# Kernel tuning notes

Measured on AMD Instinct MI355X. Metric: run time of the kernel, lower is better.

The kernel has to match this reference:

```python
import jax, jax.numpy as jnp
import numpy as np

B, DIM, H, W = 4, 512, 64, 64
HEADS = 8
MAX_FREQ = 10000.0


def _rope_cos_sin(h, w, head_dim, dtype):
    # 2D RoPE: first quarter of half_dim uses row position, second quarter uses col position
    half = head_dim // 2
    quarter = half // 2
    pos_h = jnp.arange(h, dtype=dtype)
    pos_w = jnp.arange(w, dtype=dtype)
    gh, gw = jnp.meshgrid(pos_h, pos_w, indexing='ij')
    pos = jnp.stack([gh.ravel(), gw.ravel()], axis=-1)  # [N, 2]
    freqs = 1.0 / (MAX_FREQ ** (jnp.arange(quarter, dtype=dtype) / quarter))  # [quarter]
    ang_x = pos[:, 0:1] * freqs  # [N, quarter]
    ang_y = pos[:, 1:2] * freqs  # [N, quarter]
    cos = jnp.concatenate([jnp.cos(ang_x), jnp.cos(ang_y)], axis=-1)  # [N, half]
    sin = jnp.concatenate([jnp.sin(ang_x), jnp.sin(ang_y)], axis=-1)  # [N, half]
    return cos, sin


def _apply_rope(x, cos, sin):
    # x: [B, heads, N, head_dim]; cos/sin: [N, head_dim//2]
    d = x.shape[-1] // 2
    x1, x2 = x[..., :d], x[..., d:]
    return jnp.concatenate([x1 * cos - x2 * sin, x1 * sin + x2 * cos], axis=-1)


def setup_inputs() -> dict:
    key = jax.random.key(0)
    kx, kq, kp = jax.random.split(key, 3)
    x = jax.random.normal(kx, (B, DIM, H, W), dtype=jnp.float32)
    w_qkv = jax.random.normal(kq, (3 * DIM, DIM), dtype=jnp.float32) * (DIM ** -0.5)
    w_proj = jax.random.normal(kp, (DIM, DIM), dtype=jnp.float32) * (DIM ** -0.5)
    return {"x": x, "w_qkv": w_qkv, "w_proj": w_proj}


def reference(x, w_qkv, w_proj):
    Bb, C, Hh, Ww = x.shape
    heads = HEADS
    hd = C // heads
    N = Hh * Ww
    # 1x1 conv (bias-free) == channel-wise linear
    qkv = jnp.einsum('bchw,oc->bohw', x, w_qkv)  # [B, 3C, H, W]
    qkv = qkv.reshape(Bb, 3, heads, hd, Hh, Ww).transpose(1, 0, 2, 4, 5, 3)  # [3, B, heads, H, W, hd]
    q = qkv[0].reshape(Bb, heads, N, hd)
    k = qkv[1].reshape(Bb, heads, N, hd)
    v = qkv[2].reshape(Bb, heads, N, hd)
    cos, sin = _rope_cos_sin(Hh, Ww, hd, x.dtype)
    q = _apply_rope(q, cos, sin)
    k = _apply_rope(k, cos, sin)
    scale = hd ** -0.5
    attn = jax.nn.softmax(jnp.einsum('bhnd,bhmd->bhnm', q, k) * scale, axis=-1)  # [B, heads, N, N]
    out = jnp.einsum('bhnm,bhmd->bhnd', attn, v)  # [B, heads, N, hd]
    out = out.reshape(Bb, heads, Hh, Ww, hd).transpose(0, 1, 4, 2, 3).reshape(Bb, C, Hh, Ww)
    return jnp.einsum('bchw,oc->bohw', out, w_proj)
```

## Files before the change

### kernel.cpp

```cpp
#include <hip/hip_runtime.h>
#include <math.h>

#define B_    4
#define CDIM  512
#define HEADS 8
#define HD    64
#define NN    4096
#define QSZ   ((size_t)B_*HEADS*NN*HD)
#define SCALE_Q 0.18033688011112042f

typedef __attribute__((ext_vector_type(8))) short short8;
typedef __attribute__((ext_vector_type(4))) float f32x4;
typedef __attribute__((ext_vector_type(16))) float f32x16;
union U4S8 { uint4 u; short8 s; };

__device__ inline unsigned pk(float a, float b) {
    unsigned ua = __float_as_uint(a), ub = __float_as_uint(b);
    ua += 0x7FFFu + ((ua >> 16) & 1u);
    ub += 0x7FFFu + ((ub >> 16) & 1u);
    return (ua >> 16) | (ub & 0xFFFF0000u);
}
__device__ inline unsigned short bf16_1(float a) {
    unsigned ua = __float_as_uint(a);
    ua += 0x7FFFu + ((ua >> 16) & 1u);
    return (unsigned short)(ua >> 16);
}
__device__ inline unsigned cvtpk(float a, float b) {
    unsigned r;
    asm("v_cvt_pk_bf16_f32 %0, %1, %2" : "=v"(r) : "v"(a), "v"(b));
    return r;
}

__device__ inline void load_lds16(const unsigned short* g, unsigned short* l) {
    __builtin_amdgcn_global_load_lds(
        (const __attribute__((address_space(1))) unsigned int*)g,
        (__attribute__((address_space(3))) unsigned int*)l, 16, 0, 0);
}

__global__ void conv_w_kernel(const float* __restrict__ wq, const float* __restrict__ wp,
                              unsigned short* __restrict__ wqb, unsigned short* __restrict__ wpb) {
    int id = blockIdx.x * 256 + threadIdx.x;
    const float* src; unsigned short* dst; size_t off; float sc = 1.0f;
    if (id < 98304) { src = wq; dst = wqb; off = (size_t)id * 8; if (off < 262144) sc = SCALE_Q; }
    else            { src = wp; dst = wpb; off = (size_t)(id - 98304) * 8; }
    float4 a = *(const float4*)(src + off);
    float4 b = *(const float4*)(src + off + 4);
    uint4 u;
    u.x = pk(a.x * sc, a.y * sc); u.y = pk(a.z * sc, a.w * sc);
    u.z = pk(b.x * sc, b.y * sc); u.w = pk(b.z * sc, b.w * sc);
    *(uint4*)(dst + off) = u;
}

__global__ void rope_table_kernel(float* __restrict__ ct, float* __restrict__ st) {
    int id = blockIdx.x * 256 + threadIdx.x;
    int j = id >> 12, n = id & 4095;
    int i = j & 15;
    float pos = (j < 16) ? (float)(n >> 6) : (float)(n & 63);
    float freq = exp2f(-(float)i * 0.8304820237218406f);
    float ang = pos * freq;
    ct[id] = cosf(ang);
    st[id] = sinf(ang);
}

__global__ __launch_bounds__(256) void transpose_x_kernel(
        const float* __restrict__ x, unsigned short* __restrict__ xt) {
    __shared__ unsigned short T[64 * 72];
    int t = threadIdx.x;
    int b = blockIdx.z, c0 = blockIdx.y * 64, n0 = blockIdx.x * 64;
    const float* xb = x + ((size_t)b * CDIM + c0) * NN + n0;
    int crow = t >> 2, nseg = t & 3;
#pragma unroll
    for (int g = 0; g < 4; ++g) {
        float4 f = *(const float4*)(xb + (size_t)crow * NN + nseg * 16 + g * 4);
        int nb = nseg * 16 + g * 4;
        T[(nb + 0) * 72 + crow] = bf16_1(f.x);
        T[(nb + 1) * 72 + crow] = bf16_1(f.y);
        T[(nb + 2) * 72 + crow] = bf16_1(f.z);
        T[(nb + 3) * 72 + crow] = bf16_1(f.w);
    }
    __syncthreads();
    unsigned short* xo = xt + ((size_t)b * NN + n0) * CDIM + c0;
    int nrow = t >> 2, cseg = t & 3;
    uint4 u0 = *(uint4*)(T + nrow * 72 + cseg * 16);
    uint4 u1 = *(uint4*)(T + nrow * 72 + cseg * 16 + 8);
    *(uint4*)(xo + (size_t)nrow * CDIM + cseg * 16)     = u0;
    *(uint4*)(xo + (size_t)nrow * CDIM + cseg * 16 + 8) = u1;
}

__global__ __launch_bounds__(256, 2) void qkv_mfma_kernel(
        const unsigned short* __restrict__ xt, const unsigned short* __restrict__ wq,
        unsigned short* __restrict__ qbf, unsigned short* __restrict__ kbf,
        unsigned short* __restrict__ vt,
        const float* __restrict__ ct, const float* __restrict__ st) {
    __shared__ unsigned short smem[8192];
    int t = threadIdx.x;
    int lane = t & 63, w = t >> 6;
    int qlo = lane & 15, quad = lane >> 4;
    int b = blockIdx.z, o0 = blockIdx.y * 128, n0 = blockIdx.x * 128;
    const unsigned short* xb = xt + (size_t)b * NN * CDIM;
    int row = t >> 2, seg = t & 3;
    int wn = (w & 1) * 64, wo = (w >> 1) * 64;

    f32x4 acc[4][4];
#pragma unroll
    for (int i = 0; i < 4; ++i)
#pragma unroll
        for (int j = 0; j < 4; ++j) acc[i][j] = f32x4{0.f, 0.f, 0.f, 0.f};

    for (int k0 = 0; k0 < 512; k0 += 32) {
        __syncthreads();
        load_lds16(xb + (size_t)(n0 + row) * 512 + k0 + seg * 8,        smem + t * 8);
        load_lds16(xb + (size_t)(n0 + 64 + row) * 512 + k0 + seg * 8,   smem + 2048 + t * 8);
        load_lds16(wq + (size_t)(o0 + row) * 512 + k0 + seg * 8,        smem + 4096 + t * 8);
        load_lds16(wq + (size_t)(o0 + 64 + row) * 512 + k0 + seg * 8,   smem + 6144 + t * 8);
        __syncthreads();
        U4S8 af[4], bf[4];
#pragma unroll
        for (int mt = 0; mt < 4; ++mt)
            af[mt].u = *(const uint4*)(smem + (wn + 16 * mt + qlo) * 32 + quad * 8);
#pragma unroll
        for (int nt = 0; nt < 4; ++nt)
            bf[nt].u = *(const uint4*)(smem + 4096 + (wo + 16 * nt + qlo) * 32 + quad * 8);
#pragma unroll
        for (int mt = 0; mt < 4; ++mt)
#pragma unroll
            for (int nt = 0; nt < 4; ++nt)
                acc[mt][nt] = __builtin_amdgcn_mfma_f32_16x16x32_bf16(
                    af[mt].s, bf[nt].s, acc[mt][nt], 0, 0, 0);
    }

    int og = o0 + wo;
    int s = og >> 9;
    int h = (og & 511) >> 6;
    int bh = b * HEADS + h;
    if (s < 2) {
        unsigned short* dst = (s ? kbf : qbf) + (size_t)bh * NN * HD;
#pragma unroll
        for (int mt = 0; mt < 4; ++mt) {
            int nbase = n0 + wn + 16 * mt + 4 * quad;
#pragma unroll
            for (int ntp = 0; ntp < 2; ++ntp) {
                int j = 16 * ntp + qlo;
                float4 c4 = *(const float4*)(ct + (size_t)j * NN + nbase);
                float4 s4 = *(const float4*)(st + (size_t)j * NN + nbase);
                float cc[4] = {c4.x, c4.y, c4.z, c4.w};
                float ss[4] = {s4.x, s4.y, s4.z, s4.w};
#pragma unroll
                for (int r = 0; r < 4; ++r) {
                    float x1 = acc[mt][ntp][r], x2 = acc[mt][ntp + 2][r];
                    size_t base = (size_t)(nbase + r) * HD;
                    dst[base + j]      = bf16_1(x1 * cc[r] - x2 * ss[r]);
                    dst[base + j + 32] = bf16_1(x1 * ss[r] + x2 * cc[r]);
                }
            }
        }
    } else {
        unsigned short* dst = vt + (size_t)bh * HD * NN;
#pragma unroll
        for (int mt = 0; mt < 4; ++mt)
#pragma unroll
            for (int nt = 0; nt < 4; ++nt) {
                int d = 16 * nt + qlo;
                int n = n0 + wn + 16 * mt + 4 * quad;
                uint2 u;
                u.x = pk(acc[mt][nt][0], acc[mt][nt][1]);
                u.y = pk(acc[mt][nt][2], acc[mt][nt][3]);
                *(uint2*)(dst + (size_t)d * NN + n) = u;
            }
    }
}

__global__ __launch_bounds__(256, 2) void attn_kernel(
        const unsigned short* __restrict__ qbf, const unsigned short* __restrict__ kbf,
        const unsigned short* __restrict__ vt, unsigned short* __restrict__ aot) {
    __shared__ unsigned char smem[18432];
    int t = threadIdx.x;
    int lane = t & 63, w = t >> 6;
    int l31 = lane & 31, h = lane >> 5;
    int bb = blockIdx.z, hh = blockIdx.y;
    int bh = bb * HEADS + hh;
    int n0w = blockIdx.x * 256 + w * 64;

    U4S8 qf[2][4];
    const unsigned short* qg = qbf + ((size_t)bh * NN + n0w) * HD;
#pragma unroll
    for (int mtq = 0; mtq < 2; ++mtq)
#pragma unroll
        for (int ks = 0; ks < 4; ++ks)
            qf[mtq][ks].u = *(const uint4*)(qg + (size_t)(32 * mtq + l31) * 64 + 16 * ks + 8 * h);

    short8 vone;
#pragma unroll
    for (int i = 0; i < 8; ++i) vone[i] = (short)0x3F80;

    f32x16 Zv;
#pragma unroll
    for (int i = 0; i < 16; ++i) Zv[i] = 0.f;

    f32x16 O[2][2];
#pragma unroll
    for (int mtq = 0; mtq < 2; ++mtq)
#pragma unroll
        for (int ntd = 0; ntd < 2; ++ntd) O[mtq][ntd] = Zv;
    f32x16 Lacc[2];
    Lacc[0] = Zv; Lacc[1] = Zv;

    const uint4* kg = (const uint4*)kbf + (size_t)bh * NN * 8;
    const uint4* vg = (const uint4*)vt  + (size_t)bh * 64 * 512;

    int rr0 = t >> 3, s8 = t & 7;
    int voff = 32 * (s8 >> 1) + 8 * (s8 & 1);
    uint4 kr0, kr1, vr0, vr1;
    kr0 = kg[(size_t)rr0 * 8 + s8];
    kr1 = kg[(size_t)(32 + rr0) * 8 + s8];
    vr0 = vg[(size_t)rr0 * 512 + s8];
    vr1 = vg[(size_t)(32 + rr0) * 512 + s8];

    for (int c = 0; c < NN / 64; ++c) {
        __syncthreads();
        *(uint4*)(smem + rr0 * 144 + s8 * 16)        = kr0;
        *(uint4*)(smem + (32 + rr0) * 144 + s8 * 16) = kr1;
        *(uint2*)(smem + 9216 + rr0 * 144 + voff)             = make_uint2(vr0.x, vr0.y);
        *(uint2*)(smem + 9216 + rr0 * 144 + voff + 16)        = make_uint2(vr0.z, vr0.w);
        *(uint2*)(smem + 9216 + (32 + rr0) * 144 + voff)      = make_uint2(vr1.x, vr1.y);
        *(uint2*)(smem + 9216 + (32 + rr0) * 144 + voff + 16) = make_uint2(vr1.z, vr1.w);
        __syncthreads();
        if (c + 1 < NN / 64) {
            int m0 = (c + 1) * 64;
            kr0 = kg[(size_t)(m0 + rr0) * 8 + s8];
            kr1 = kg[(size_t)(m0 + 32 + rr0) * 8 + s8];
            vr0 = vg[(size_t)rr0 * 512 + (m0 >> 3) + s8];
            vr1 = vg[(size_t)(32 + rr0) * 512 + (m0 >> 3) + s8];
        }

#pragma unroll
        for (int mtk = 0; mtk < 2; ++mtk) {
            U4S8 ka[4];
#pragma unroll
            for (int ks = 0; ks < 4; ++ks)
                ka[ks].u = *(const uint4*)(smem + (32 * mtk + l31) * 144 + 32 * ks + 16 * h);
            f32x16 S[2];
            __builtin_amdgcn_s_setprio(1);
#pragma unroll
            for (int mtq = 0; mtq < 2; ++mtq) {
                S[mtq] = __builtin_amdgcn_mfma_f32_32x32x16_bf16(
                    ka[0].s, qf[mtq][0].s, Zv, 0, 0, 0);
#pragma unroll
                for (int ks = 1; ks < 4; ++ks)
                    S[mtq] = __builtin_amdgcn_mfma_f32_32x32x16_bf16(
                        ka[ks].s, qf[mtq][ks].s, S[mtq], 0, 0, 0);
            }
            __builtin_amdgcn_s_setprio(0);

            U4S8 pa[2][2];
#pragma unroll
            for (int mtq = 0; mtq < 2; ++mtq) {
                float p[16];
#pragma unroll
                for (int r = 0; r < 16; ++r) p[r] = __builtin_amdgcn_exp2f(S[mtq][r]);
#pragma unroll
                for (int ksl = 0; ksl < 2; ++ksl) {
                    pa[ksl][mtq].u.x = cvtpk(p[8 * ksl + 0], p[8 * ksl + 1]);
                    pa[ksl][mtq].u.y = cvtpk(p[8 * ksl + 2], p[8 * ksl + 3]);
                    pa[ksl][mtq].u.z = cvtpk(p[8 * ksl + 4], p[8 * ksl + 5]);
                    pa[ksl][mtq].u.w = cvtpk(p[8 * ksl + 6], p[8 * ksl + 7]);
                }
            }

            __builtin_amdgcn_s_setprio(1);
#pragma unroll
            for (int ksl = 0; ksl < 2; ++ksl) {
#pragma unroll
                for (int mtq = 0; mtq < 2; ++mtq)
                    Lacc[mtq] = __builtin_amdgcn_mfma_f32_32x32x16_bf16(
                        pa[ksl][mtq].s, vone, Lacc[mtq], 0, 0, 0);
#pragma unroll
                for (int ntd = 0; ntd < 2; ++ntd) {
                    U4S8 vb;
                    vb.u = *(const uint4*)(smem + 9216 + (32 * ntd + l31) * 144
                                           + 64 * mtk + 32 * ksl + 16 * h);
#pragma unroll
                    for (int mtq = 0; mtq < 2; ++mtq)
                        O[mtq][ntd] = __builtin_amdgcn_mfma_f32_32x32x16_bf16(
                            pa[ksl][mtq].s, vb.s, O[mtq][ntd], 0, 0, 0);
                }
            }
            __builtin_amdgcn_s_setprio(0);
        }
    }

    __syncthreads();
    unsigned short* Tw = (unsigned short*)(smem + w * 4608);
    unsigned short* aob = aot + ((size_t)bb * NN) * CDIM + hh * 64;
#pragma unroll
    for (int mtq = 0; mtq < 2; ++mtq) {
        float iv[16];
#pragma unroll
        for (int r = 0; r < 16; ++r) iv[r] = 1.0f / Lacc[mtq][r];
#pragma unroll
        for (int rg = 0; rg < 2; ++rg) {
#pragma unroll
            for (int ntd = 0; ntd < 2; ++ntd)
#pragma unroll
                for (int rr = 0; rr < 8; ++rr) {
                    int r = 8 * rg + rr;
                    int q16 = (rr & 3) + 8 * (rr >> 2) + 4 * h;
                    Tw[q16 * 72 + 32 * ntd + l31] = bf16_1(O[mtq][ntd][r] * iv[r]);
                }
            int row = lane >> 2, cseg = lane & 3;
            uint4 u0 = *(uint4*)(Tw + row * 72 + cseg * 16);
            uint4 u1 = *(uint4*)(Tw + row * 72 + cseg * 16 + 8);
            unsigned short* arow = aob
                + (size_t)(n0w + 32 * mtq + 16 * rg + row) * CDIM + cseg * 16;
            *(uint4*)(arow)     = u0;
            *(uint4*)(arow + 8) = u1;
        }
    }
}

__global__ __launch_bounds__(256, 2) void proj_mfma_kernel(
        const unsigned short* __restrict__ aot, const unsigned short* __restrict__ wp,
        float* __restrict__ out) {
    __shared__ unsigned short smem[8192];
    int t = threadIdx.x;
    int lane = t & 63, w = t >> 6;
    int qlo = lane & 15, quad = lane >> 4;
    int b = blockIdx.z, o0 = blockIdx.y * 128, n0 = blockIdx.x * 128;
    const unsigned short* ab = aot + (size_t)b * NN * CDIM;
    int row = t >> 2, seg = t & 3;
    int wn = (w & 1) * 64, wo = (w >> 1) * 64;

    f32x4 acc[4][4];
#pragma unroll
    for (int i = 0; i < 4; ++i)
#pragma unroll
        for (int j = 0; j < 4; ++j) acc[i][j] = f32x4{0.f, 0.f, 0.f, 0.f};

    for (int k0 = 0; k0 < 512; k0 += 32) {
        __syncthreads();
        load_lds16(ab + (size_t)(n0 + row) * 512 + k0 + seg * 8,        smem + t * 8);
        load_lds16(ab + (size_t)(n0 + 64 + row) * 512 + k0 + seg * 8,   smem + 2048 + t * 8);
        load_lds16(wp + (size_t)(o0 + row) * 512 + k0 + seg * 8,        smem + 4096 + t * 8);
        load_lds16(wp + (size_t)(o0 + 64 + row) * 512 + k0 + seg * 8,   smem + 6144 + t * 8);
        __syncthreads();
        U4S8 af[4], bf[4];
#pragma unroll
        for (int mt = 0; mt < 4; ++mt)
            af[mt].u = *(const uint4*)(smem + (wn + 16 * mt + qlo) * 32 + quad * 8);
#pragma unroll
        for (int nt = 0; nt < 4; ++nt)
            bf[nt].u = *(const uint4*)(smem + 4096 + (wo + 16 * nt + qlo) * 32 + quad * 8);
#pragma unroll
        for (int mt = 0; mt < 4; ++mt)
#pragma unroll
            for (int nt = 0; nt < 4; ++nt)
                acc[mt][nt] = __builtin_amdgcn_mfma_f32_16x16x32_bf16(
                    af[mt].s, bf[nt].s, acc[mt][nt], 0, 0, 0);
    }

    float* ob = out + (size_t)b * CDIM * NN;
#pragma unroll
    for (int mt = 0; mt < 4; ++mt)
#pragma unroll
        for (int nt = 0; nt < 4; ++nt) {
            int o = o0 + wo + 16 * nt + qlo;
            int n = n0 + wn + 16 * mt + 4 * quad;
            *(float4*)(ob + (size_t)o * NN + n) = *(float4*)&acc[mt][nt];
        }
}

extern "C" void kernel_launch(void* const* d_in, const int* in_sizes, int n_in,
                              void* d_out, int out_size, void* d_ws, size_t ws_size,
                              hipStream_t stream) {
    const float* x      = (const float*)d_in[0];
    const float* w_qkv  = (const float*)d_in[1];
    const float* w_proj = (const float*)d_in[2];
    float* out = (float*)d_out;
    unsigned short* ws = (unsigned short*)d_ws;

    unsigned short* xt  = ws;
    unsigned short* qbf = xt  + QSZ;
    unsigned short* kbf = qbf + QSZ;
    unsigned short* vt  = kbf + QSZ;
    unsigned short* aot = vt  + QSZ;
    unsigned short* wqb = aot + QSZ;
    unsigned short* wpb = wqb + 786432;
    float* ct = (float*)(wpb + 262144);
    float* st = ct + 32 * 4096;

    conv_w_kernel<<<512, 256, 0, stream>>>(w_qkv, w_proj, wqb, wpb);
    rope_table_kernel<<<512, 256, 0, stream>>>(ct, st);
    transpose_x_kernel<<<dim3(64, 8, B_), 256, 0, stream>>>(x, xt);
    qkv_mfma_kernel<<<dim3(32, 12, B_), 256, 0, stream>>>(xt, wqb, qbf, kbf, vt, ct, st);
    attn_kernel<<<dim3(NN / 256, HEADS, B_), 256, 0, stream>>>(qbf, kbf, vt, aot);
    proj_mfma_kernel<<<dim3(32, 4, B_), 256, 0, stream>>>(aot, wpb, out);
}
```

Measured before the change: 293.7 us.

## Replace ones-vector MFMA row-sum with scalar accumulation and restructure S tile loop

Removes the MFMA that multiplied P by a ones vector to get the softmax denominator. Each lane now sums its exp values in scalar registers, combines halves with a cross-lane shuffle at the end, and redistributes the reciprocals to the output row layout via shuffles. The QK^T loop is also reordered to compute both key sub-tiles (S[2][2]) at once before exp and PV. This cuts matrix-core work per tile, but adds VALU adds, uses the fp32 rather than bf16-rounded P for the sum, and keeps more live registers.

```diff
diff --git a/kernel.cpp b/kernel.cpp
--- a/kernel.cpp
+++ b/kernel.cpp
@@ -189,10 +189,6 @@
         for (int ks = 0; ks < 4; ++ks)
             qf[mtq][ks].u = *(const uint4*)(qg + (size_t)(32 * mtq + l31) * 64 + 16 * ks + 8 * h);
 
-    short8 vone;
-#pragma unroll
-    for (int i = 0; i < 8; ++i) vone[i] = (short)0x3F80;
-
     f32x16 Zv;
 #pragma unroll
     for (int i = 0; i < 16; ++i) Zv[i] = 0.f;
@@ -202,8 +198,7 @@
     for (int mtq = 0; mtq < 2; ++mtq)
 #pragma unroll
         for (int ntd = 0; ntd < 2; ++ntd) O[mtq][ntd] = Zv;
-    f32x16 Lacc[2];
-    Lacc[0] = Zv; Lacc[1] = Zv;
+    float Lsum[2] = {0.f, 0.f};
 
     const uint4* kg = (const uint4*)kbf + (size_t)bh * NN * 8;
     const uint4* vg = (const uint4*)vt  + (size_t)bh * 64 * 512;
@@ -233,47 +228,62 @@
             vr1 = vg[(size_t)(32 + rr0) * 512 + (m0 >> 3) + s8];
         }
 
-#pragma unroll
-        for (int mtk = 0; mtk < 2; ++mtk) {
-            U4S8 ka[4];
-#pragma unroll
-            for (int ks = 0; ks < 4; ++ks)
-                ka[ks].u = *(const uint4*)(smem + (32 * mtk + l31) * 144 + 32 * ks + 16 * h);
-            f32x16 S[2];
-            __builtin_amdgcn_s_setprio(1);
-#pragma unroll
-            for (int mtq = 0; mtq < 2; ++mtq) {
-                S[mtq] = __builtin_amdgcn_mfma_f32_32x32x16_bf16(
-                    ka[0].s, qf[mtq][0].s, Zv, 0, 0, 0);
-#pragma unroll
-                for (int ks = 1; ks < 4; ++ks)
-                    S[mtq] = __builtin_amdgcn_mfma_f32_32x32x16_bf16(
-                        ka[ks].s, qf[mtq][ks].s, S[mtq], 0, 0, 0);
+        f32x16 S[2][2];
+        __builtin_amdgcn_s_setprio(1);
+        {
+            U4S8 ka0[2];
+#pragma unroll
+            for (int mtk = 0; mtk < 2; ++mtk)
+                ka0[mtk].u = *(const uint4*)(smem + (32 * mtk + l31) * 144 + 16 * h);
+#pragma unroll
+            for (int mtk = 0; mtk < 2; ++mtk)
+#pragma unroll
+                for (int mtq = 0; mtq < 2; ++mtq)
+                    S[mtk][mtq] = __builtin_amdgcn_mfma_f32_32x32x16_bf16(
+                        ka0[mtk].s, qf[mtq][0].s, Zv, 0, 0, 0);
+#pragma unroll
+            for (int ks = 1; ks < 4; ++ks) {
+                U4S8 ka[2];
+#pragma unroll
+                for (int mtk = 0; mtk < 2; ++mtk)
+                    ka[mtk].u = *(const uint4*)(smem + (32 * mtk + l31) * 144 + 32 * ks + 16 * h);
+#pragma unroll
+                for (int mtk = 0; mtk < 2; ++mtk)
+#pragma unroll
+                    for (int mtq = 0; mtq < 2; ++mtq)
+                        S[mtk][mtq] = __builtin_amdgcn_mfma_f32_32x32x16_bf16(
+                            ka[mtk].s, qf[mtq][ks].s, S[mtk][mtq], 0, 0, 0);
             }
-            __builtin_amdgcn_s_setprio(0);
-
-            U4S8 pa[2][2];
-#pragma unroll
-            for (int mtq = 0; mtq < 2; ++mtq) {
-                float p[16];
-#pragma unroll
-                for (int r = 0; r < 16; ++r) p[r] = __builtin_amdgcn_exp2f(S[mtq][r]);
+        }
+        __builtin_amdgcn_s_setprio(0);
+
+        U4S8 pa[2][2][2];
+#pragma unroll
+        for (int mtk = 0; mtk < 2; ++mtk)
+#pragma unroll
+            for (int mtq = 0; mtq < 2; ++mtq)
 #pragma unroll
                 for (int ksl = 0; ksl < 2; ++ksl) {
-                    pa[ksl][mtq].u.x = cvtpk(p[8 * ksl + 0], p[8 * ksl + 1]);
-                    pa[ksl][mtq].u.y = cvtpk(p[8 * ksl + 2], p[8 * ksl + 3]);
-                    pa[ksl][mtq].u.z = cvtpk(p[8 * ksl + 4], p[8 * ksl + 5]);
-                    pa[ksl][mtq].u.w = cvtpk(p[8 * ksl + 6], p[8 * ksl + 7]);
+                    float p0 = __builtin_amdgcn_exp2f(S[mtk][mtq][8 * ksl + 0]);
+                    float p1 = __builtin_amdgcn_exp2f(S[mtk][mtq][8 * ksl + 1]);
+                    float p2 = __builtin_amdgcn_exp2f(S[mtk][mtq][8 * ksl + 2]);
+                    float p3 = __builtin_amdgcn_exp2f(S[mtk][mtq][8 * ksl + 3]);
+                    float p4 = __builtin_amdgcn_exp2f(S[mtk][mtq][8 * ksl + 4]);
+                    float p5 = __builtin_amdgcn_exp2f(S[mtk][mtq][8 * ksl + 5]);
+                    float p6 = __builtin_amdgcn_exp2f(S[mtk][mtq][8 * ksl + 6]);
+                    float p7 = __builtin_amdgcn_exp2f(S[mtk][mtq][8 * ksl + 7]);
+                    Lsum[mtq] += ((p0 + p1) + (p2 + p3)) + ((p4 + p5) + (p6 + p7));
+                    pa[mtk][ksl][mtq].u.x = cvtpk(p0, p1);
+                    pa[mtk][ksl][mtq].u.y = cvtpk(p2, p3);
+                    pa[mtk][ksl][mtq].u.z = cvtpk(p4, p5);
+                    pa[mtk][ksl][mtq].u.w = cvtpk(p6, p7);
                 }
-            }
-
-            __builtin_amdgcn_s_setprio(1);
-#pragma unroll
-            for (int ksl = 0; ksl < 2; ++ksl) {
-#pragma unroll
-                for (int mtq = 0; mtq < 2; ++mtq)
-                    Lacc[mtq] = __builtin_amdgcn_mfma_f32_32x32x16_bf16(
-                        pa[ksl][mtq].s, vone, Lacc[mtq], 0, 0, 0);
+
+        __builtin_amdgcn_s_setprio(1);
+#pragma unroll
+        for (int mtk = 0; mtk < 2; ++mtk)
+#pragma unroll
+            for (int ksl = 0; ksl < 2; ++ksl)
 #pragma unroll
                 for (int ntd = 0; ntd < 2; ++ntd) {
                     U4S8 vb;
@@ -282,13 +292,17 @@
 #pragma unroll
                     for (int mtq = 0; mtq < 2; ++mtq)
                         O[mtq][ntd] = __builtin_amdgcn_mfma_f32_32x32x16_bf16(
-                            pa[ksl][mtq].s, vb.s, O[mtq][ntd], 0, 0, 0);
+                            pa[mtk][ksl][mtq].s, vb.s, O[mtq][ntd], 0, 0, 0);
                 }
-            }
-            __builtin_amdgcn_s_setprio(0);
-        }
-    }
-
+        __builtin_amdgcn_s_setprio(0);
+    }
+
+    float Linv[2];
+#pragma unroll
+    for (int mtq = 0; mtq < 2; ++mtq) {
+        float l = Lsum[mtq] + __shfl_xor(Lsum[mtq], 32, 64);
+        Linv[mtq] = 1.0f / l;
+    }
     __syncthreads();
     unsigned short* Tw = (unsigned short*)(smem + w * 4608);
     unsigned short* aob = aot + ((size_t)bb * NN) * CDIM + hh * 64;
@@ -296,7 +310,10 @@
     for (int mtq = 0; mtq < 2; ++mtq) {
         float iv[16];
 #pragma unroll
-        for (int r = 0; r < 16; ++r) iv[r] = 1.0f / Lacc[mtq][r];
+        for (int r = 0; r < 16; ++r) {
+            int src = (r & 3) + 8 * ((r >> 2) & 1) + 16 * (r >> 3) + 4 * h;
+            iv[r] = __shfl(Linv[mtq], src, 64);
+        }
 #pragma unroll
         for (int rg = 0; rg < 2; ++rg) {
 #pragma unroll
```

Result: no change. 291.9 us (-0.6%).
